# Kernel tuning notes

Measured on AMD Instinct MI355X. Metric: run time of the kernel, lower is better.

The kernel has to match this reference:

```python
import jax, jax.numpy as jnp
import numpy as np

NOOBJ_LAMBDA = 0.5
COORD_LAMBDA = 5.0


def _cxcywh_to_xyxy(b):
    cx, cy, w, h = b[..., 0], b[..., 1], b[..., 2], b[..., 3]
    return jnp.stack([cx - w / 2, cy - h / 2, cx + w / 2, cy + h / 2], axis=-1)


def _pairwise_iou(a, b):
    # a: [B, N, 4] xyxy (preds), b: [B, M, 4] xyxy (targets) -> [B, N, M]
    lt = jnp.maximum(a[:, :, None, :2], b[:, None, :, :2])
    rb = jnp.minimum(a[:, :, None, 2:], b[:, None, :, 2:])
    wh = jnp.clip(rb - lt, 0.0)
    inter = wh[..., 0] * wh[..., 1]
    area_a = (a[..., 2] - a[..., 0]) * (a[..., 3] - a[..., 1])
    area_b = (b[..., 2] - b[..., 0]) * (b[..., 3] - b[..., 1])
    union = area_a[:, :, None] + area_b[:, None, :] - inter
    return inter / jnp.where(union > 0, union, 1.0)


def setup_inputs() -> dict:
    key = jax.random.key(0)
    kp, kt, km = jax.random.split(key, 3)
    B = 8192
    # positive values so sqrt(w), sqrt(h) is well-defined (as the torch code assumes)
    pred = jax.random.uniform(kp, (B, 7, 7, 30), dtype=jnp.float32, minval=0.05, maxval=1.0)
    target = jax.random.uniform(kt, (B, 7, 7, 30), dtype=jnp.float32, minval=0.05, maxval=1.0)
    # target confidence channel (index 4) is the obj/noobj indicator: 0 or 1
    obj = (jax.random.uniform(km, (B, 7, 7)) < 0.2).astype(jnp.float32)
    target = target.at[..., 4].set(obj)
    return {"pred_tensor": pred, "target_tensor": target}


def reference(pred_tensor, target_tensor):
    B = pred_tensor.shape[0]
    pred = pred_tensor.reshape(B, 49, 30)
    target = target_tensor.reshape(B, 49, 30)

    conf_t = target[..., 4]            # [B,49]
    noobj = conf_t == 0                # [B,49]
    obj = conf_t > 0                   # [B,49]

    # --- no-object confidence loss (channels 4 and 9) ---
    d4 = pred[..., 4] - target[..., 4]
    d9 = pred[..., 9] - target[..., 9]
    noobj_loss = jnp.sum(jnp.where(noobj, d4 * d4 + d9 * d9, 0.0))

    # --- object cells: 2 boxes per cell, padded to all 49 cells with a mask ---
    pb = pred[..., :10].reshape(B, 98, 5)
    tb = target[..., :10].reshape(B, 98, 5)
    box_mask = jnp.repeat(obj, 2, axis=1)  # [B,98]

    p_xyxy = _cxcywh_to_xyxy(pb[..., :4])
    t_xyxy = _cxcywh_to_xyxy(tb[..., :4])
    iou = _pairwise_iou(p_xyxy, t_xyxy)  # [B,98,98]
    pair_mask = box_mask[:, :, None] & box_mask[:, None, :]
    iou = jnp.where(pair_mask, iou, 0.0)
    max_iou = jnp.max(iou, axis=1)       # max over pred boxes, per target box [B,98]
    cmask = (max_iou != 0) & box_mask    # [B,98]

    cm = cmask.astype(pred.dtype)
    # coord (cx,cy) loss
    dxy = pb[..., :2] - tb[..., :2]
    coord_loss_cxcy = jnp.sum(cm * jnp.sum(dxy * dxy, axis=-1))
    # coord (sqrt w, sqrt h) loss
    dwh = jnp.sqrt(pb[..., 2:4]) - jnp.sqrt(tb[..., 2:4])
    coord_loss_wh = jnp.sum(cm * jnp.sum(dwh * dwh, axis=-1))
    # object confidence loss
    dconf = pb[..., 4] - tb[..., 4]
    obj_loss = jnp.sum(cm * dconf * dconf)

    # --- class loss over object cells ---
    dcls = pred[..., 10:] - target[..., 10:]
    cls_loss = jnp.sum(obj.astype(pred.dtype) * jnp.sum(dcls * dcls, axis=-1))

    bsz = jnp.asarray(B, pred.dtype)
    batch_cls_loss = cls_loss / bsz
    batch_obj_loss = (obj_loss + noobj_loss * NOOBJ_LAMBDA) / bsz
    batch_coord_loss = (coord_loss_cxcy + coord_loss_wh) * COORD_LAMBDA / bsz
    batch_loss = batch_cls_loss + batch_obj_loss + batch_coord_loss
    return (batch_loss, batch_cls_loss, batch_obj_loss, batch_coord_loss)
```

## Files before the change

### kernel.cpp

```cpp
#include <hip/hip_runtime.h>

#define CH 30
#define CELLS 49
#define ROW (CELLS * CH)
#define RPB 4

__device__ __forceinline__ float waveReduce(float v) {
    #pragma unroll
    for (int o = 32; o > 0; o >>= 1) v += __shfl_xor(v, o, 64);
    return v;
}

__global__ __launch_bounds__(256) void yolo_main(const float* __restrict__ pred,
                                                 const float* __restrict__ targ,
                                                 float* __restrict__ ws,
                                                 int B, int NB) {
    const int w = threadIdx.x >> 6;
    const int lane = threadIdx.x & 63;
    const int r = blockIdx.x * RPB + w;
    const bool rowOk = (r < B);

    __shared__ float spb[RPB][CELLS * 10];
    __shared__ float stb[RPB][CELLS * 10];
    __shared__ float4 boxS[RPB][2 * CELLS];
    __shared__ int clist[RPB][CELLS];
    __shared__ float partial[RPB][3];

    const float* P = pred + (size_t)r * ROW;
    const float* T = targ + (size_t)r * ROW;

    bool isObj = false;
    if (rowOk && lane < CELLS) isObj = T[lane * CH + 4] > 0.f;
    const unsigned long long mask = __ballot(isObj);
    const int nObj = __popcll(mask);
    if (isObj) {
        const int pos = __popcll(mask & ((1ull << lane) - 1ull));
        clist[w][pos] = lane;
    }

    float cls = 0.f, objc = 0.f, coord = 0.f;

    if (rowOk) {
        const float2* P2 = (const float2*)P;
        const float2* T2 = (const float2*)T;
        for (int j = lane; j < ROW / 2; j += 64) {
            const float2 p = P2[j];
            const float2 t = T2[j];
            const int cell = j / 15;
            const int ch0 = 2 * (j - cell * 15);
            const bool obj = (mask >> cell) & 1ull;
            if (ch0 >= 10) {
                if (obj) {
                    const float dx = p.x - t.x, dy = p.y - t.y;
                    cls += dx * dx + dy * dy;
                }
            } else if (obj) {
                *(float2*)&spb[w][cell * 10 + ch0] = p;
                *(float2*)&stb[w][cell * 10 + ch0] = t;
            } else {
                if (ch0 == 4) objc += 0.5f * p.x * p.x;
                else if (ch0 == 8) { const float d = p.y - t.y; objc += 0.5f * d * d; }
            }
        }
    }
    __syncthreads();

    const int nBox = 2 * nObj;

    for (int e = lane; e < nBox; e += 64) {
        const int c = clist[w][e >> 1];
        const float* pb = &spb[w][c * 10 + (e & 1) * 5];
        const float cx = pb[0], cy = pb[1], bw = pb[2], bh = pb[3];
        boxS[w][e] = make_float4(cx - 0.5f * bw, cy - 0.5f * bh,
                                 cx + 0.5f * bw, cy + 0.5f * bh);
    }
    __syncthreads();

    for (int e = lane; e < nBox; e += 64) {
        const int c = clist[w][e >> 1];
        const int bb = c * 10 + (e & 1) * 5;
        const float tcx = stb[w][bb], tcy = stb[w][bb + 1];
        const float tw = stb[w][bb + 2], th = stb[w][bb + 3];
        const float tx1 = tcx - 0.5f * tw, ty1 = tcy - 0.5f * th;
        const float tx2 = tcx + 0.5f * tw, ty2 = tcy + 0.5f * th;
        const float ta = (tx2 - tx1) * (ty2 - ty1);
        float maxiou = 0.f;
        for (int i = 0; i < nBox; ++i) {
            const float4 pb4 = boxS[w][i];
            const float lx = fmaxf(pb4.x, tx1), ly = fmaxf(pb4.y, ty1);
            const float rx = fminf(pb4.z, tx2), ry = fminf(pb4.w, ty2);
            const float iw = fmaxf(rx - lx, 0.f), ih = fmaxf(ry - ly, 0.f);
            const float inter = iw * ih;
            const float pa = (pb4.z - pb4.x) * (pb4.w - pb4.y);
            const float un = pa + ta - inter;
            const float iou = inter / (un > 0.f ? un : 1.f);
            maxiou = fmaxf(maxiou, iou);
        }
        if (maxiou != 0.f) {
            const float dcx = spb[w][bb] - tcx, dcy = spb[w][bb + 1] - tcy;
            coord += dcx * dcx + dcy * dcy;
            const float dw = sqrtf(spb[w][bb + 2]) - sqrtf(tw);
            const float dh = sqrtf(spb[w][bb + 3]) - sqrtf(th);
            coord += dw * dw + dh * dh;
            const float dc = spb[w][bb + 4] - stb[w][bb + 4];
            objc += dc * dc;
        }
    }

    cls = waveReduce(cls); objc = waveReduce(objc); coord = waveReduce(coord);
    if (lane == 0) { partial[w][0] = cls; partial[w][1] = objc; partial[w][2] = coord; }
    __syncthreads();
    if (threadIdx.x == 0) {
        float c = 0.f, o = 0.f, x = 0.f;
        #pragma unroll
        for (int i = 0; i < RPB; ++i) { c += partial[i][0]; o += partial[i][1]; x += partial[i][2]; }
        ws[blockIdx.x] = c;
        ws[NB + blockIdx.x] = o;
        ws[2 * NB + blockIdx.x] = x;
    }
}

__global__ __launch_bounds__(1024) void yolo_reduce(const float* __restrict__ ws,
                                                    float* __restrict__ out,
                                                    int NB, float invB) {
    const int tid = threadIdx.x;
    const int w = tid >> 6, lane = tid & 63;
    __shared__ float sred[16];
    __shared__ float sums[3];
    #pragma unroll
    for (int s = 0; s < 3; ++s) {
        float v = 0.f;
        for (int i = tid; i < NB; i += 1024) v += ws[s * NB + i];
        v = waveReduce(v);
        if (lane == 0) sred[w] = v;
        __syncthreads();
        if (tid == 0) {
            float t = 0.f;
            #pragma unroll
            for (int k = 0; k < 16; ++k) t += sred[k];
            sums[s] = t;
        }
        __syncthreads();
    }
    if (tid == 0) {
        const float bcls = sums[0] * invB;
        const float bobj = sums[1] * invB;
        const float bcoord = sums[2] * 5.0f * invB;
        out[0] = bcls + bobj + bcoord;
        out[1] = bcls;
        out[2] = bobj;
        out[3] = bcoord;
    }
}

extern "C" void kernel_launch(void* const* d_in, const int* in_sizes, int n_in,
                              void* d_out, int out_size, void* d_ws, size_t ws_size,
                              hipStream_t stream) {
    const float* pred = (const float*)d_in[0];
    const float* targ = (const float*)d_in[1];
    float* ws = (float*)d_ws;
    float* out = (float*)d_out;
    const int B = in_sizes[0] / ROW;
    const int NB = (B + RPB - 1) / RPB;

    yolo_main<<<NB, 256, 0, stream>>>(pred, targ, ws, B, NB);
    yolo_reduce<<<1, 1024, 0, stream>>>(ws, out, NB, 1.0f / (float)B);
}
```

Before: 133.2 us.

## Batch row loads branch-free and drop shared staging of box channels

The streaming loop now issues all twelve float2 loads per lane up front, in two halves of six with clamped indices, and computes class and no-object losses with predicated arithmetic instead of divergent branches. The cell index comes from a multiply-shift in place of division. Box data is no longer copied into shared memory; the IoU and coord phases re-read pred and target from global memory, relying on cache hits. Per-row partial sums go straight to the workspace, removing the block-level shared reduction and its barrier, at the cost of a larger final reduction over B entries.

```diff
diff --git a/kernel.cpp b/kernel.cpp
--- a/kernel.cpp
+++ b/kernel.cpp
@@ -2,8 +2,10 @@
 
 #define CH 30
 #define CELLS 49
-#define ROW (CELLS * CH)
+#define ROW 1470
 #define RPB 4
+#define NPAIR 735
+#define HALF 6
 
 __device__ __forceinline__ float waveReduce(float v) {
     #pragma unroll
@@ -13,24 +15,19 @@
 
 __global__ __launch_bounds__(256) void yolo_main(const float* __restrict__ pred,
                                                  const float* __restrict__ targ,
-                                                 float* __restrict__ ws,
-                                                 int B, int NB) {
+                                                 float* __restrict__ ws, int B) {
     const int w = threadIdx.x >> 6;
     const int lane = threadIdx.x & 63;
     const int r = blockIdx.x * RPB + w;
     const bool rowOk = (r < B);
 
-    __shared__ float spb[RPB][CELLS * 10];
-    __shared__ float stb[RPB][CELLS * 10];
     __shared__ float4 boxS[RPB][2 * CELLS];
     __shared__ int clist[RPB][CELLS];
-    __shared__ float partial[RPB][3];
 
     const float* P = pred + (size_t)r * ROW;
     const float* T = targ + (size_t)r * ROW;
 
-    bool isObj = false;
-    if (rowOk && lane < CELLS) isObj = T[lane * CH + 4] > 0.f;
+    bool isObj = rowOk && (lane < CELLS) && (T[lane * CH + 4] > 0.f);
     const unsigned long long mask = __ballot(isObj);
     const int nObj = __popcll(mask);
     if (isObj) {
@@ -40,26 +37,32 @@
 
     float cls = 0.f, objc = 0.f, coord = 0.f;
 
+    const float2* P2 = (const float2*)P;
+    const float2* T2 = (const float2*)T;
     if (rowOk) {
-        const float2* P2 = (const float2*)P;
-        const float2* T2 = (const float2*)T;
-        for (int j = lane; j < ROW / 2; j += 64) {
-            const float2 p = P2[j];
-            const float2 t = T2[j];
-            const int cell = j / 15;
-            const int ch0 = 2 * (j - cell * 15);
-            const bool obj = (mask >> cell) & 1ull;
-            if (ch0 >= 10) {
-                if (obj) {
-                    const float dx = p.x - t.x, dy = p.y - t.y;
-                    cls += dx * dx + dy * dy;
-                }
-            } else if (obj) {
-                *(float2*)&spb[w][cell * 10 + ch0] = p;
-                *(float2*)&stb[w][cell * 10 + ch0] = t;
-            } else {
-                if (ch0 == 4) objc += 0.5f * p.x * p.x;
-                else if (ch0 == 8) { const float d = p.y - t.y; objc += 0.5f * d * d; }
+        #pragma unroll
+        for (int h = 0; h < 2; ++h) {
+            float2 pv[HALF], tv[HALF];
+            #pragma unroll
+            for (int it = 0; it < HALF; ++it) {
+                const int j = lane + (h * HALF + it) * 64;
+                const int jc = j < NPAIR ? j : NPAIR - 1;
+                pv[it] = P2[jc];
+                tv[it] = T2[jc];
+            }
+            #pragma unroll
+            for (int it = 0; it < HALF; ++it) {
+                const int j = lane + (h * HALF + it) * 64;
+                const bool valid = j < NPAIR;
+                const int cell = (j * 17477) >> 18;
+                const int ch0 = 2 * (j - cell * 15);
+                const float wobj = (float)((mask >> cell) & 1ull);
+                const float dx = pv[it].x - tv[it].x;
+                const float dy = pv[it].y - tv[it].y;
+                const float ss = dx * dx + dy * dy;
+                cls += (valid && ch0 >= 10) ? wobj * ss : 0.f;
+                const float nn = (ch0 == 4 ? dx * dx : 0.f) + (ch0 == 8 ? dy * dy : 0.f);
+                objc += valid ? 0.5f * (1.f - wobj) * nn : 0.f;
             }
         }
     }
@@ -69,7 +72,7 @@
 
     for (int e = lane; e < nBox; e += 64) {
         const int c = clist[w][e >> 1];
-        const float* pb = &spb[w][c * 10 + (e & 1) * 5];
+        const float* pb = P + c * CH + (e & 1) * 5;
         const float cx = pb[0], cy = pb[1], bw = pb[2], bh = pb[3];
         boxS[w][e] = make_float4(cx - 0.5f * bw, cy - 0.5f * bh,
                                  cx + 0.5f * bw, cy + 0.5f * bh);
@@ -78,9 +81,8 @@
 
     for (int e = lane; e < nBox; e += 64) {
         const int c = clist[w][e >> 1];
-        const int bb = c * 10 + (e & 1) * 5;
-        const float tcx = stb[w][bb], tcy = stb[w][bb + 1];
-        const float tw = stb[w][bb + 2], th = stb[w][bb + 3];
+        const float* tb = T + c * CH + (e & 1) * 5;
+        const float tcx = tb[0], tcy = tb[1], tw = tb[2], th = tb[3];
         const float tx1 = tcx - 0.5f * tw, ty1 = tcy - 0.5f * th;
         const float tx2 = tcx + 0.5f * tw, ty2 = tcy + 0.5f * th;
         const float ta = (tx2 - tx1) * (ty2 - ty1);
@@ -97,32 +99,28 @@
             maxiou = fmaxf(maxiou, iou);
         }
         if (maxiou != 0.f) {
-            const float dcx = spb[w][bb] - tcx, dcy = spb[w][bb + 1] - tcy;
+            const float* pb = P + c * CH + (e & 1) * 5;
+            const float dcx = pb[0] - tcx, dcy = pb[1] - tcy;
             coord += dcx * dcx + dcy * dcy;
-            const float dw = sqrtf(spb[w][bb + 2]) - sqrtf(tw);
-            const float dh = sqrtf(spb[w][bb + 3]) - sqrtf(th);
+            const float dw = sqrtf(pb[2]) - sqrtf(tw);
+            const float dh = sqrtf(pb[3]) - sqrtf(th);
             coord += dw * dw + dh * dh;
-            const float dc = spb[w][bb + 4] - stb[w][bb + 4];
+            const float dc = pb[4] - tb[4];
             objc += dc * dc;
         }
     }
 
     cls = waveReduce(cls); objc = waveReduce(objc); coord = waveReduce(coord);
-    if (lane == 0) { partial[w][0] = cls; partial[w][1] = objc; partial[w][2] = coord; }
-    __syncthreads();
-    if (threadIdx.x == 0) {
-        float c = 0.f, o = 0.f, x = 0.f;
-        #pragma unroll
-        for (int i = 0; i < RPB; ++i) { c += partial[i][0]; o += partial[i][1]; x += partial[i][2]; }
-        ws[blockIdx.x] = c;
-        ws[NB + blockIdx.x] = o;
-        ws[2 * NB + blockIdx.x] = x;
+    if (rowOk && lane == 0) {
+        ws[r] = cls;
+        ws[B + r] = objc;
+        ws[2 * B + r] = coord;
     }
 }
 
 __global__ __launch_bounds__(1024) void yolo_reduce(const float* __restrict__ ws,
                                                     float* __restrict__ out,
-                                                    int NB, float invB) {
+                                                    int B, float invB) {
     const int tid = threadIdx.x;
     const int w = tid >> 6, lane = tid & 63;
     __shared__ float sred[16];
@@ -130,7 +128,7 @@
     #pragma unroll
     for (int s = 0; s < 3; ++s) {
         float v = 0.f;
-        for (int i = tid; i < NB; i += 1024) v += ws[s * NB + i];
+        for (int i = tid; i < B; i += 1024) v += ws[s * B + i];
         v = waveReduce(v);
         if (lane == 0) sred[w] = v;
         __syncthreads();
@@ -163,6 +161,6 @@
     const int B = in_sizes[0] / ROW;
     const int NB = (B + RPB - 1) / RPB;
 
-    yolo_main<<<NB, 256, 0, stream>>>(pred, targ, ws, B, NB);
-    yolo_reduce<<<1, 1024, 0, stream>>>(ws, out, NB, 1.0f / (float)B);
+    yolo_main<<<NB, 256, 0, stream>>>(pred, targ, ws, B);
+    yolo_reduce<<<1, 1024, 0, stream>>>(ws, out, B, 1.0f / (float)B);
 }
```

Measured after the change: 127.0 us. 1.05x faster.
